# Kernel optimization log

Hardware: AMD Instinct MI355X
Metric: run time of the kernel (lower is better)

The kernel has to match this reference:

```python
import jax, jax.numpy as jnp
import numpy as np

N_NODES = 100000
N_EDGES = 3200000
NUM_FEATURES = 256
HIDDEN = 16
NUM_CLASSES = 40


def gcn_conv(x, edge_index, W, b, num_nodes):
    """PyG GCNConv: linear -> add self-loops -> symmetric deg norm -> scatter-add -> bias."""
    x = x @ W  # [N, out]
    loop = jnp.arange(num_nodes)
    src = jnp.concatenate([edge_index[0], loop])  # messages flow src -> dst
    dst = jnp.concatenate([edge_index[1], loop])
    # degree of target nodes (with self-loops)
    deg = jax.ops.segment_sum(jnp.ones_like(dst, dtype=x.dtype), dst,
                              num_segments=num_nodes)
    dinv = jnp.where(deg > 0, jax.lax.rsqrt(deg), 0.0)
    norm = dinv[src] * dinv[dst]  # [E+N]
    out = jax.ops.segment_sum(x[src] * norm[:, None], dst,
                              num_segments=num_nodes)
    return out + b


def setup_inputs() -> dict:
    key = jax.random.key(0)
    k1, k2, k3, k4 = jax.random.split(key, 4)
    x = jax.random.normal(k1, (N_NODES, NUM_FEATURES), dtype=jnp.float32)
    edge_index = jax.random.randint(k2, (2, N_EDGES), 0, N_NODES, dtype=jnp.int64)
    W1 = jax.random.normal(k3, (NUM_FEATURES, HIDDEN), dtype=jnp.float32) / np.sqrt(NUM_FEATURES)
    b1 = jnp.zeros((HIDDEN,), dtype=jnp.float32)
    W2 = jax.random.normal(k4, (HIDDEN, NUM_CLASSES), dtype=jnp.float32) / np.sqrt(HIDDEN)
    b2 = jnp.zeros((NUM_CLASSES,), dtype=jnp.float32)
    return {"x": x, "edge_index": edge_index, "W1": W1, "b1": b1, "W2": W2, "b2": b2}


def reference(x, edge_index, W1, b1, W2, b2):
    h = jax.nn.relu(gcn_conv(x, edge_index, W1, b1, N_NODES))
    return gcn_conv(h, edge_index, W2, b2, N_NODES)
```

## Files before the change

kernel.cpp:

```cpp
#include <hip/hip_runtime.h>
#include <hip/hip_fp16.h>

#define N_NODES   100000
#define N_EDGES   3200000
#define F_IN      256
#define HID       16
#define NCLS      40

#define CHUNK     16384
#define NBLK      ((N_EDGES + CHUNK - 1) / CHUNK)
#define B2SHIFT   9
#define NB2       ((N_NODES + 511) >> B2SHIFT)
#define BCAP      17408
#define K1_GRID   256
#define NPB       391

__global__ __launch_bounds__(512) void k1_hist_gemm(const int* __restrict__ ei,
                                                    const float* __restrict__ x,
                                                    const float* __restrict__ W1,
                                                    int* __restrict__ hist_blk,
                                                    __half* __restrict__ y1h) {
    __shared__ float W1s[F_IN * HID];
    int* h = (int*)W1s;
    int blk = blockIdx.x, t = threadIdx.x;

    if (blk < NBLK) {
        for (int i = t; i < NB2; i += 512) h[i] = 0;
        __syncthreads();
        int e0 = blk * CHUNK;
        int eN = min(CHUNK, N_EDGES - e0);
        const int4* d4 = (const int4*)(ei + N_EDGES + e0);
        for (int i = t; i < (eN >> 2); i += 512) {
            int4 d = d4[i];
            atomicAdd(&h[d.x >> B2SHIFT], 1);
            atomicAdd(&h[d.y >> B2SHIFT], 1);
            atomicAdd(&h[d.z >> B2SHIFT], 1);
            atomicAdd(&h[d.w >> B2SHIFT], 1);
        }
        __syncthreads();
        for (int i = t; i < NB2; i += 512) hist_blk[i * NBLK + blk] = h[i];
        __syncthreads();
    }

    #pragma unroll
    for (int i = 0; i < (F_IN * HID) / 512; i++) W1s[t + i * 512] = W1[t + i * 512];
    __syncthreads();

    int n = blk * NPB + t;
    if (t >= NPB || n >= N_NODES) return;

    const float4* xr = (const float4*)(x + (size_t)n * F_IN);
    float acc[HID];
    #pragma unroll
    for (int j = 0; j < HID; j++) acc[j] = 0.f;

    #pragma unroll 4
    for (int k4 = 0; k4 < F_IN / 4; k4++) {
        float4 xv = xr[k4];
        int k = k4 * 4;
        #pragma unroll
        for (int hh = 0; hh < HID; hh++) {
            acc[hh] += xv.x * W1s[(k + 0) * HID + hh] + xv.y * W1s[(k + 1) * HID + hh]
                     + xv.z * W1s[(k + 2) * HID + hh] + xv.w * W1s[(k + 3) * HID + hh];
        }
    }
    __half2 hp[8];
    #pragma unroll
    for (int j = 0; j < 8; j++)
        hp[j] = __float22half2_rn(make_float2(acc[2 * j], acc[2 * j + 1]));
    float4* o = (float4*)(y1h + (size_t)n * HID);
    o[0] = ((float4*)hp)[0];
    o[1] = ((float4*)hp)[1];
}

__global__ __launch_bounds__(512) void k2_bin(const int* __restrict__ ei,
                                              const int* __restrict__ hist_blk,
                                              int* __restrict__ buf) {
    __shared__ int cur[NB2];
    __shared__ int sc[256];
    int blk = blockIdx.x, t = threadIdx.x;
    int pre = 0, tot = 0;
    if (t < NB2) {
        const int* row = hist_blk + t * NBLK;
        for (int k = 0; k < NBLK; k++) {
            int v = row[k];
            pre += (k < blk) ? v : 0;
            tot += v;
        }
    }
    if (t < 256) sc[t] = tot;
    __syncthreads();
    for (int off = 1; off < 256; off <<= 1) {
        int u = 0;
        if (t < 256 && t >= off) u = sc[t - off];
        __syncthreads();
        if (t < 256) sc[t] += u;
        __syncthreads();
    }
    if (t < NB2) cur[t] = (sc[t] - tot) + pre;
    __syncthreads();

    int e0 = blk * CHUNK;
    int eN = min(CHUNK, N_EDGES - e0);
    const int4* s4 = (const int4*)(ei + e0);
    const int4* d4 = (const int4*)(ei + N_EDGES + e0);
    for (int i = t; i < (eN >> 2); i += 512) {
        int4 d = d4[i], s = s4[i];
        int p0 = atomicAdd(&cur[d.x >> B2SHIFT], 1); buf[p0] = ((d.x & 511) << 17) | s.x;
        int p1 = atomicAdd(&cur[d.y >> B2SHIFT], 1); buf[p1] = ((d.y & 511) << 17) | s.y;
        int p2 = atomicAdd(&cur[d.z >> B2SHIFT], 1); buf[p2] = ((d.z & 511) << 17) | s.z;
        int p3 = atomicAdd(&cur[d.w >> B2SHIFT], 1); buf[p3] = ((d.w & 511) << 17) | s.w;
    }
}

__global__ __launch_bounds__(512) void k3_build(const int* __restrict__ buf,
                                               const int* __restrict__ hist_blk,
                                               int* __restrict__ rowptr,
                                               float* __restrict__ dinv,
                                               int* __restrict__ csr_src) {
    __shared__ int lbuf[BCAP];
    __shared__ int hist[512], offs[512], cur[512];
    __shared__ int sc[256];
    __shared__ int s_base, s_cnt;
    int b = blockIdx.x, t = threadIdx.x;

    int tot = 0;
    if (t < NB2) {
        const int* row = hist_blk + t * NBLK;
        for (int k = 0; k < NBLK; k++) tot += row[k];
    }
    if (t < 256) sc[t] = tot;
    hist[t] = 0;
    __syncthreads();
    for (int off = 1; off < 256; off <<= 1) {
        int u = 0;
        if (t < 256 && t >= off) u = sc[t - off];
        __syncthreads();
        if (t < 256) sc[t] += u;
        __syncthreads();
    }
    if (t == b) { s_base = sc[b] - tot; s_cnt = tot; }
    __syncthreads();
    int base = s_base, cnt = s_cnt;

    for (int i = t; i < cnt; i += 512) {
        int v = buf[base + i];
        if (i < BCAP) lbuf[i] = v;
        atomicAdd(&hist[v >> 17], 1);
    }
    __syncthreads();
    int v = hist[t];
    offs[t] = v;
    __syncthreads();
    for (int off = 1; off < 512; off <<= 1) {
        int u = (t >= off) ? offs[t - off] : 0;
        __syncthreads();
        offs[t] += u;
        __syncthreads();
    }
    int ex = offs[t] - v;
    int n = (b << B2SHIFT) + t;
    if (n < N_NODES) {
        rowptr[n] = base + ex;
        dinv[n]   = rsqrtf((float)(v + 1));
    }
    if (b == 0 && t == 0) rowptr[N_NODES] = N_EDGES;
    cur[t] = ex;
    __syncthreads();
    for (int i = t; i < cnt; i += 512) {
        int p = (i < BCAP) ? lbuf[i] : buf[base + i];
        int pos = atomicAdd(&cur[p >> 17], 1);
        csr_src[base + pos] = p & 0x1FFFF;
    }
}

__device__ __forceinline__ void acc_row_s(const float4* __restrict__ tab, int s, float w, float* acc) {
    float4 v0 = tab[(size_t)s * 2 + 0];
    float4 v1 = tab[(size_t)s * 2 + 1];
    const __half2* a0 = (const __half2*)&v0;
    const __half2* a1 = (const __half2*)&v1;
    #pragma unroll
    for (int j = 0; j < 4; j++) {
        float2 f0 = __half22float2(a0[j]);
        float2 f1 = __half22float2(a1[j]);
        acc[2 * j]         += w * f0.x;
        acc[2 * j + 1]     += w * f0.y;
        acc[8 + 2 * j]     += w * f1.x;
        acc[8 + 2 * j + 1] += w * f1.y;
    }
}

__device__ __forceinline__ void acc_row2_s(const float4* __restrict__ tab, int s0, int s1,
                                           float w0, float w1, float* acc) {
    float4 v0 = tab[(size_t)s0 * 2 + 0];
    float4 v1 = tab[(size_t)s0 * 2 + 1];
    float4 v2 = tab[(size_t)s1 * 2 + 0];
    float4 v3 = tab[(size_t)s1 * 2 + 1];
    const __half2* a0 = (const __half2*)&v0;
    const __half2* a1 = (const __half2*)&v1;
    const __half2* b0 = (const __half2*)&v2;
    const __half2* b1 = (const __half2*)&v3;
    #pragma unroll
    for (int j = 0; j < 4; j++) {
        float2 f0 = __half22float2(a0[j]);
        float2 f1 = __half22float2(a1[j]);
        float2 g0 = __half22float2(b0[j]);
        float2 g1 = __half22float2(b1[j]);
        acc[2 * j]         += w0 * f0.x + w1 * g0.x;
        acc[2 * j + 1]     += w0 * f0.y + w1 * g0.y;
        acc[8 + 2 * j]     += w0 * f1.x + w1 * g1.x;
        acc[8 + 2 * j + 1] += w0 * f1.y + w1 * g1.y;
    }
}

__device__ __forceinline__ void acc_row(const float4* __restrict__ tab, int s, float* acc) {
    float4 v0 = tab[(size_t)s * 2 + 0];
    float4 v1 = tab[(size_t)s * 2 + 1];
    const __half2* a0 = (const __half2*)&v0;
    const __half2* a1 = (const __half2*)&v1;
    #pragma unroll
    for (int j = 0; j < 4; j++) {
        float2 f0 = __half22float2(a0[j]);
        float2 f1 = __half22float2(a1[j]);
        acc[2 * j]         += f0.x;
        acc[2 * j + 1]     += f0.y;
        acc[8 + 2 * j]     += f1.x;
        acc[8 + 2 * j + 1] += f1.y;
    }
}

__device__ __forceinline__ void acc_row2(const float4* __restrict__ tab, int s0, int s1, float* acc) {
    float4 v0 = tab[(size_t)s0 * 2 + 0];
    float4 v1 = tab[(size_t)s0 * 2 + 1];
    float4 v2 = tab[(size_t)s1 * 2 + 0];
    float4 v3 = tab[(size_t)s1 * 2 + 1];
    const __half2* a0 = (const __half2*)&v0;
    const __half2* a1 = (const __half2*)&v1;
    const __half2* b0 = (const __half2*)&v2;
    const __half2* b1 = (const __half2*)&v3;
    #pragma unroll
    for (int j = 0; j < 4; j++) {
        float2 f0 = __half22float2(a0[j]);
        float2 f1 = __half22float2(a1[j]);
        float2 g0 = __half22float2(b0[j]);
        float2 g1 = __half22float2(b1[j]);
        acc[2 * j]         += f0.x + g0.x;
        acc[2 * j + 1]     += f0.y + g0.y;
        acc[8 + 2 * j]     += f1.x + g1.x;
        acc[8 + 2 * j + 1] += f1.y + g1.y;
    }
}

__global__ __launch_bounds__(256) void gather1_kernel(const int* __restrict__ rowptr,
                                                      const int* __restrict__ csr_src,
                                                      const __half* __restrict__ y1h,
                                                      const float* __restrict__ b1,
                                                      const float* __restrict__ dinv,
                                                      __half* __restrict__ zh) {
    int n   = blockIdx.x * 64 + (threadIdx.x >> 2);
    int sub = threadIdx.x & 3;
    if (n >= N_NODES) return;
    const float4* tab = (const float4*)y1h;
    float dvn = dinv[n];
    int beg = rowptr[n], end = rowptr[n + 1];
    float acc[16];
    #pragma unroll
    for (int i = 0; i < 16; i++) acc[i] = 0.f;
    if (sub == 0) acc_row_s(tab, n, dvn, acc);
    int e = beg + sub;
    for (; e + 4 < end; e += 8) {
        int s0 = csr_src[e], s1 = csr_src[e + 4];
        acc_row2_s(tab, s0, s1, dinv[s0], dinv[s1], acc);
    }
    if (e < end) {
        int s = csr_src[e];
        acc_row_s(tab, s, dinv[s], acc);
    }
    #pragma unroll
    for (int m = 1; m < 4; m <<= 1) {
        #pragma unroll
        for (int i = 0; i < 16; i++) acc[i] += __shfl_xor(acc[i], m, 4);
    }
    if (sub < 2) {
        const float4* b1q = (const float4*)b1;
        float4 ba = b1q[sub * 2], bb = b1q[sub * 2 + 1];
        float bv[8] = {ba.x, ba.y, ba.z, ba.w, bb.x, bb.y, bb.z, bb.w};
        __half2 outp[4];
        #pragma unroll
        for (int j = 0; j < 4; j++) {
            float2 r;
            r.x = fmaxf(dvn * acc[sub * 8 + 2 * j]     + bv[2 * j],     0.f) * dvn;
            r.y = fmaxf(dvn * acc[sub * 8 + 2 * j + 1] + bv[2 * j + 1], 0.f) * dvn;
            outp[j] = __float22half2_rn(r);
        }
        *(float4*)(zh + (size_t)n * HID + sub * 8) = *(float4*)outp;
    }
}

__global__ __launch_bounds__(256) void gather2_kernel(const int* __restrict__ rowptr,
                                                      const int* __restrict__ csr_src,
                                                      const __half* __restrict__ zh,
                                                      const float* __restrict__ W2,
                                                      const float* __restrict__ b2,
                                                      const float* __restrict__ dinv,
                                                      float* __restrict__ out) {
    __shared__ float W2s[HID * NCLS];
    __shared__ float b2s[NCLS];
    int t = threadIdx.x;
    for (int i = t; i < HID * NCLS; i += 256) W2s[i] = W2[i];
    if (t < NCLS) b2s[t] = b2[t];
    __syncthreads();

    int n   = blockIdx.x * 64 + (t >> 2);
    int sub = t & 3;
    if (n >= N_NODES) return;
    const float4* tab = (const float4*)zh;
    int beg = rowptr[n], end = rowptr[n + 1];
    float acc[16];
    #pragma unroll
    for (int i = 0; i < 16; i++) acc[i] = 0.f;
    if (sub == 0) acc_row(tab, n, acc);
    int e = beg + sub;
    for (; e + 4 < end; e += 8)
        acc_row2(tab, csr_src[e], csr_src[e + 4], acc);
    if (e < end) acc_row(tab, csr_src[e], acc);
    #pragma unroll
    for (int m = 1; m < 4; m <<= 1) {
        #pragma unroll
        for (int i = 0; i < 16; i++) acc[i] += __shfl_xor(acc[i], m, 4);
    }
    float dv = dinv[n];
    int c0 = sub * 10;
    float o[10];
    #pragma unroll
    for (int j = 0; j < 10; j++) o[j] = 0.f;
    #pragma unroll
    for (int h = 0; h < HID; h++) {
        float a = acc[h];
        const float* w = &W2s[h * NCLS + c0];
        #pragma unroll
        for (int j = 0; j < 10; j++) o[j] += a * w[j];
    }
    float* op = out + (size_t)n * NCLS + c0;
    #pragma unroll
    for (int j = 0; j < 5; j++) {
        float2 r = make_float2(dv * o[2 * j]     + b2s[c0 + 2 * j],
                               dv * o[2 * j + 1] + b2s[c0 + 2 * j + 1]);
        *(float2*)(op + 2 * j) = r;
    }
}

extern "C" void kernel_launch(void* const* d_in, const int* in_sizes, int n_in,
                              void* d_out, int out_size, void* d_ws, size_t ws_size,
                              hipStream_t stream) {
    const float* x   = (const float*)d_in[0];
    const int*   ei  = (const int*)  d_in[1];
    const float* W1  = (const float*)d_in[2];
    const float* b1  = (const float*)d_in[3];
    const float* W2  = (const float*)d_in[4];
    const float* b2  = (const float*)d_in[5];
    float* out = (float*)d_out;

    char* ws = (char*)d_ws;
    size_t off = 0;
    int*   hist_blk = (int*)(ws + off); off += (size_t)NB2 * NBLK * 4;
    off = (off + 15) & ~(size_t)15;
    int*    rowptr  = (int*)   (ws + off); off += (size_t)(N_NODES + 1) * 4;
    off = (off + 15) & ~(size_t)15;
    float*  dinv    = (float*) (ws + off); off += (size_t)N_NODES * 4;
    int*    csr_src = (int*)   (ws + off); off += (size_t)N_EDGES * 4;
    int*    buf     = (int*)   (ws + off); off += (size_t)N_EDGES * 4;
    __half* y1h     = (__half*)(ws + off); off += (size_t)N_NODES * HID * 2;
    __half* zh      = (__half*)(ws + off); off += (size_t)N_NODES * HID * 2;

    k1_hist_gemm <<<K1_GRID, 512, 0, stream>>>(ei, x, W1, hist_blk, y1h);
    k2_bin       <<<NBLK, 512, 0, stream>>>(ei, hist_blk, buf);
    k3_build     <<<NB2, 512, 0, stream>>>(buf, hist_blk, rowptr, dinv, csr_src);
    gather1_kernel<<<(N_NODES + 63) / 64, 256, 0, stream>>>(rowptr, csr_src, y1h, b1, dinv, zh);
    gather2_kernel<<<(N_NODES + 63) / 64, 256, 0, stream>>>(rowptr, csr_src, zh, W2, b2, dinv, out);
}
```

Measured before the change: 337.4 us.

## Prescale layer-1 features by dinv in build kernel; retile GEMM to two rows per thread

```diff
diff --git a/kernel.cpp b/kernel.cpp
--- a/kernel.cpp
+++ b/kernel.cpp
@@ -12,10 +12,8 @@
 #define B2SHIFT   9
 #define NB2       ((N_NODES + 511) >> B2SHIFT)
 #define BCAP      17408
-#define K1_GRID   256
-#define NPB       391
-
-__global__ __launch_bounds__(512) void k1_hist_gemm(const int* __restrict__ ei,
+
+__global__ __launch_bounds__(256) void k1_hist_gemm(const int* __restrict__ ei,
                                                     const float* __restrict__ x,
                                                     const float* __restrict__ W1,
                                                     int* __restrict__ hist_blk,
@@ -24,53 +22,70 @@
     int* h = (int*)W1s;
     int blk = blockIdx.x, t = threadIdx.x;
 
-    if (blk < NBLK) {
-        for (int i = t; i < NB2; i += 512) h[i] = 0;
-        __syncthreads();
-        int e0 = blk * CHUNK;
-        int eN = min(CHUNK, N_EDGES - e0);
-        const int4* d4 = (const int4*)(ei + N_EDGES + e0);
-        for (int i = t; i < (eN >> 2); i += 512) {
-            int4 d = d4[i];
-            atomicAdd(&h[d.x >> B2SHIFT], 1);
-            atomicAdd(&h[d.y >> B2SHIFT], 1);
-            atomicAdd(&h[d.z >> B2SHIFT], 1);
-            atomicAdd(&h[d.w >> B2SHIFT], 1);
+    for (int i = t; i < NB2; i += 256) h[i] = 0;
+    __syncthreads();
+    int e0 = blk * CHUNK;
+    int eN = min(CHUNK, N_EDGES - e0);
+    const int4* d4 = (const int4*)(ei + N_EDGES + e0);
+    for (int i = t; i < (eN >> 2); i += 256) {
+        int4 d = d4[i];
+        atomicAdd(&h[d.x >> B2SHIFT], 1);
+        atomicAdd(&h[d.y >> B2SHIFT], 1);
+        atomicAdd(&h[d.z >> B2SHIFT], 1);
+        atomicAdd(&h[d.w >> B2SHIFT], 1);
+    }
+    __syncthreads();
+    for (int i = t; i < NB2; i += 256) hist_blk[i * NBLK + blk] = h[i];
+    __syncthreads();
+
+    #pragma unroll
+    for (int i = 0; i < (F_IN * HID) / 256; i++) W1s[t + i * 256] = W1[t + i * 256];
+    __syncthreads();
+
+    int n0 = blk * 512 + t;
+    int n1 = n0 + 256;
+    if (n0 >= N_NODES) return;
+    bool v1 = (n1 < N_NODES);
+
+    const float4* xr0 = (const float4*)(x + (size_t)n0 * F_IN);
+    const float4* xr1 = (const float4*)(x + (size_t)(v1 ? n1 : n0) * F_IN);
+    float acc0[HID], acc1[HID];
+    #pragma unroll
+    for (int j = 0; j < HID; j++) { acc0[j] = 0.f; acc1[j] = 0.f; }
+
+    #pragma unroll 2
+    for (int k4 = 0; k4 < F_IN / 4; k4++) {
+        float4 xa = xr0[k4];
+        float4 xb = xr1[k4];
+        int k = k4 * 4;
+        #pragma unroll
+        for (int hh = 0; hh < HID; hh++) {
+            float w0 = W1s[(k + 0) * HID + hh];
+            float w1 = W1s[(k + 1) * HID + hh];
+            float w2 = W1s[(k + 2) * HID + hh];
+            float w3 = W1s[(k + 3) * HID + hh];
+            acc0[hh] += xa.x * w0 + xa.y * w1 + xa.z * w2 + xa.w * w3;
+            acc1[hh] += xb.x * w0 + xb.y * w1 + xb.z * w2 + xb.w * w3;
         }
-        __syncthreads();
-        for (int i = t; i < NB2; i += 512) hist_blk[i * NBLK + blk] = h[i];
-        __syncthreads();
-    }
-
-    #pragma unroll
-    for (int i = 0; i < (F_IN * HID) / 512; i++) W1s[t + i * 512] = W1[t + i * 512];
-    __syncthreads();
-
-    int n = blk * NPB + t;
-    if (t >= NPB || n >= N_NODES) return;
-
-    const float4* xr = (const float4*)(x + (size_t)n * F_IN);
-    float acc[HID];
-    #pragma unroll
-    for (int j = 0; j < HID; j++) acc[j] = 0.f;
-
-    #pragma unroll 4
-    for (int k4 = 0; k4 < F_IN / 4; k4++) {
-        float4 xv = xr[k4];
-        int k = k4 * 4;
-        #pragma unroll
-        for (int hh = 0; hh < HID; hh++) {
-            acc[hh] += xv.x * W1s[(k + 0) * HID + hh] + xv.y * W1s[(k + 1) * HID + hh]
-                     + xv.z * W1s[(k + 2) * HID + hh] + xv.w * W1s[(k + 3) * HID + hh];
-        }
-    }
-    __half2 hp[8];
-    #pragma unroll
-    for (int j = 0; j < 8; j++)
-        hp[j] = __float22half2_rn(make_float2(acc[2 * j], acc[2 * j + 1]));
-    float4* o = (float4*)(y1h + (size_t)n * HID);
-    o[0] = ((float4*)hp)[0];
-    o[1] = ((float4*)hp)[1];
+    }
+    {
+        __half2 hp[8];
+        #pragma unroll
+        for (int j = 0; j < 8; j++)
+            hp[j] = __float22half2_rn(make_float2(acc0[2 * j], acc0[2 * j + 1]));
+        float4* o = (float4*)(y1h + (size_t)n0 * HID);
+        o[0] = ((float4*)hp)[0];
+        o[1] = ((float4*)hp)[1];
+    }
+    if (v1) {
+        __half2 hp[8];
+        #pragma unroll
+        for (int j = 0; j < 8; j++)
+            hp[j] = __float22half2_rn(make_float2(acc1[2 * j], acc1[2 * j + 1]));
+        float4* o = (float4*)(y1h + (size_t)n1 * HID);
+        o[0] = ((float4*)hp)[0];
+        o[1] = ((float4*)hp)[1];
+    }
 }
 
 __global__ __launch_bounds__(512) void k2_bin(const int* __restrict__ ei,
@@ -117,7 +132,8 @@
                                                const int* __restrict__ hist_blk,
                                                int* __restrict__ rowptr,
                                                float* __restrict__ dinv,
-                                               int* __restrict__ csr_src) {
+                                               int* __restrict__ csr_src,
+                                               __half* __restrict__ y1h) {
     __shared__ int lbuf[BCAP];
     __shared__ int hist[512], offs[512], cur[512];
     __shared__ int sc[256];
@@ -162,7 +178,21 @@
     int n = (b << B2SHIFT) + t;
     if (n < N_NODES) {
         rowptr[n] = base + ex;
-        dinv[n]   = rsqrtf((float)(v + 1));
+        float dv = rsqrtf((float)(v + 1));
+        dinv[n] = dv;
+        float4* yr = (float4*)(y1h + (size_t)n * HID);
+        float4 a = yr[0], bqq = yr[1];
+        __half2* ah = (__half2*)&a;
+        __half2* bh = (__half2*)&bqq;
+        #pragma unroll
+        for (int j = 0; j < 4; j++) {
+            float2 fa = __half22float2(ah[j]);
+            float2 fb = __half22float2(bh[j]);
+            ah[j] = __float22half2_rn(make_float2(fa.x * dv, fa.y * dv));
+            bh[j] = __float22half2_rn(make_float2(fb.x * dv, fb.y * dv));
+        }
+        yr[0] = a;
+        yr[1] = bqq;
     }
     if (b == 0 && t == 0) rowptr[N_NODES] = N_EDGES;
     cur[t] = ex;
@@ -171,45 +201,6 @@
         int p = (i < BCAP) ? lbuf[i] : buf[base + i];
         int pos = atomicAdd(&cur[p >> 17], 1);
         csr_src[base + pos] = p & 0x1FFFF;
-    }
-}
-
-__device__ __forceinline__ void acc_row_s(const float4* __restrict__ tab, int s, float w, float* acc) {
-    float4 v0 = tab[(size_t)s * 2 + 0];
-    float4 v1 = tab[(size_t)s * 2 + 1];
-    const __half2* a0 = (const __half2*)&v0;
-    const __half2* a1 = (const __half2*)&v1;
-    #pragma unroll
-    for (int j = 0; j < 4; j++) {
-        float2 f0 = __half22float2(a0[j]);
-        float2 f1 = __half22float2(a1[j]);
-        acc[2 * j]         += w * f0.x;
-        acc[2 * j + 1]     += w * f0.y;
-        acc[8 + 2 * j]     += w * f1.x;
-        acc[8 + 2 * j + 1] += w * f1.y;
-    }
-}
-
-__device__ __forceinline__ void acc_row2_s(const float4* __restrict__ tab, int s0, int s1,
-                                           float w0, float w1, float* acc) {
-    float4 v0 = tab[(size_t)s0 * 2 + 0];
-    float4 v1 = tab[(size_t)s0 * 2 + 1];
-    float4 v2 = tab[(size_t)s1 * 2 + 0];
-    float4 v3 = tab[(size_t)s1 * 2 + 1];
-    const __half2* a0 = (const __half2*)&v0;
-    const __half2* a1 = (const __half2*)&v1;
-    const __half2* b0 = (const __half2*)&v2;
-    const __half2* b1 = (const __half2*)&v3;
-    #pragma unroll
-    for (int j = 0; j < 4; j++) {
-        float2 f0 = __half22float2(a0[j]);
-        float2 f1 = __half22float2(a1[j]);
-        float2 g0 = __half22float2(b0[j]);
-        float2 g1 = __half22float2(b1[j]);
-        acc[2 * j]         += w0 * f0.x + w1 * g0.x;
-        acc[2 * j + 1]     += w0 * f0.y + w1 * g0.y;
-        acc[8 + 2 * j]     += w0 * f1.x + w1 * g1.x;
-        acc[8 + 2 * j + 1] += w0 * f1.y + w1 * g1.y;
     }
 }
 
@@ -261,27 +252,22 @@
     int sub = threadIdx.x & 3;
     if (n >= N_NODES) return;
     const float4* tab = (const float4*)y1h;
-    float dvn = dinv[n];
     int beg = rowptr[n], end = rowptr[n + 1];
     float acc[16];
     #pragma unroll
     for (int i = 0; i < 16; i++) acc[i] = 0.f;
-    if (sub == 0) acc_row_s(tab, n, dvn, acc);
+    if (sub == 0) acc_row(tab, n, acc);
     int e = beg + sub;
-    for (; e + 4 < end; e += 8) {
-        int s0 = csr_src[e], s1 = csr_src[e + 4];
-        acc_row2_s(tab, s0, s1, dinv[s0], dinv[s1], acc);
-    }
-    if (e < end) {
-        int s = csr_src[e];
-        acc_row_s(tab, s, dinv[s], acc);
-    }
+    for (; e + 4 < end; e += 8)
+        acc_row2(tab, csr_src[e], csr_src[e + 4], acc);
+    if (e < end) acc_row(tab, csr_src[e], acc);
     #pragma unroll
     for (int m = 1; m < 4; m <<= 1) {
         #pragma unroll
         for (int i = 0; i < 16; i++) acc[i] += __shfl_xor(acc[i], m, 4);
     }
     if (sub < 2) {
+        float dvn = dinv[n];
         const float4* b1q = (const float4*)b1;
         float4 ba = b1q[sub * 2], bb = b1q[sub * 2 + 1];
         float bv[8] = {ba.x, ba.y, ba.z, ba.w, bb.x, bb.y, bb.z, bb.w};
@@ -373,9 +359,9 @@
     __half* y1h     = (__half*)(ws + off); off += (size_t)N_NODES * HID * 2;
     __half* zh      = (__half*)(ws + off); off += (size_t)N_NODES * HID * 2;
 
-    k1_hist_gemm <<<K1_GRID, 512, 0, stream>>>(ei, x, W1, hist_blk, y1h);
+    k1_hist_gemm <<<NBLK, 256, 0, stream>>>(ei, x, W1, hist_blk, y1h);
     k2_bin       <<<NBLK, 512, 0, stream>>>(ei, hist_blk, buf);
-    k3_build     <<<NB2, 512, 0, stream>>>(buf, hist_blk, rowptr, dinv, csr_src);
+    k3_build     <<<NB2, 512, 0, stream>>>(buf, hist_blk, rowptr, dinv, csr_src, y1h);
     gather1_kernel<<<(N_NODES + 63) / 64, 256, 0, stream>>>(rowptr, csr_src, y1h, b1, dinv, zh);
     gather2_kernel<<<(N_NODES + 63) / 64, 256, 0, stream>>>(rowptr, csr_src, zh, W2, b2, dinv, out);
 }
```

New measurement: 325.2 us. 1.04x faster.
